# Kernel optimization log

Measured on AMD Instinct MI355X. Metric: run time of the kernel, lower is better.

Reference implementation:

```python
import jax, jax.numpy as jnp
import numpy as np

N = 100000   # nodes
E = 1600000  # edges (avg degree 16)
F_IN, F_HID, F_OUT = 64, 64, 16


def setup_inputs() -> dict:
    key = jax.random.key(0)
    ks = jax.random.split(key, 10)
    features = jax.random.normal(ks[0], (N, F_IN), dtype=jnp.float32)
    src = jax.random.randint(ks[1], (E,), 0, N, dtype=jnp.int32)
    dst = jax.random.randint(ks[2], (E,), 0, N, dtype=jnp.int32)
    # Xavier-uniform weights, zero bias (matches nn.init in the module)
    def xavier(k, fan_in, fan_out):
        lim = np.sqrt(6.0 / (fan_in + fan_out))
        return jax.random.uniform(k, (fan_in, fan_out), jnp.float32, -lim, lim)
    return {
        "features": features,
        "W1": xavier(ks[3], F_IN, F_HID), "b1": jnp.zeros((F_HID,), jnp.float32),
        "W2": xavier(ks[4], F_HID, F_HID), "b2": jnp.zeros((F_HID,), jnp.float32),
        "W3": xavier(ks[5], F_HID, F_OUT), "b3": jnp.zeros((F_OUT,), jnp.float32),
        "src": src, "dst": dst,
    }


def pairnorm_scs(x):
    # PairNorm 'PN-SCS', scale=1
    col_mean = x.mean(axis=0)                                    # [F]
    rownorm = jnp.sqrt(1e-6 + jnp.sum(x * x, axis=1, keepdims=True))  # [N,1]
    return x / rownorm - col_mean


def graph_conv(h, src, dst, W, b):
    # copy_u('h','m') + sum reduce over edges, plus self-loop
    agg = jax.ops.segment_sum(h[src], dst, num_segments=N) + h   # [N,F]
    return agg @ W + b


def reference(features, W1, b1, W2, b2, W3, b3, src, dst):
    h = features
    for W, b in ((W1, b1), (W2, b2)):
        h = pairnorm_scs(h)
        h = jax.nn.relu(graph_conv(h, src, dst, W, b))
        # dropout p=0.0 -> identity
    return graph_conv(h, src, dst, W3, b3)
```

## Files before the change

### kernel.cpp

```cpp
#include <hip/hip_runtime.h>
#include <hip/hip_fp8.h>


#define NHB 128

__device__ __forceinline__ unsigned short f2bf(float f) {
  unsigned u = __builtin_bit_cast(unsigned, f);
  u += 0x7FFFu + ((u >> 16) & 1u);
  return (unsigned short)(u >> 16);
}
__device__ __forceinline__ float bf2f(unsigned short h) {
  return __builtin_bit_cast(float, ((unsigned)h) << 16);
}
__device__ __forceinline__ float rlane(float v, int k) {
  return __builtin_bit_cast(
      float, __builtin_amdgcn_readlane(__builtin_bit_cast(int, v), k));
}
__device__ __forceinline__ unsigned char f2fp8(float f) {
  __hip_fp8_e4m3 t(f);
  return (unsigned char)t.__x;
}
__device__ __forceinline__ float fp8tof(unsigned v) {
#if __has_builtin(__builtin_amdgcn_cvt_f32_fp8)
  return __builtin_amdgcn_cvt_f32_fp8((int)v, 0);
#else
  const unsigned h = ((v << 8) & 0x8000u) | ((v << 7) & 0x3f80u);
  __half_raw hr; hr.x = (unsigned short)h;
  return (float)__half(hr) * 256.0f;
#endif
}

__global__ __launch_bounds__(256) void prelude_kernel(
    const int* __restrict__ dst, int* __restrict__ cntA, int E,
    const float* __restrict__ x, float* __restrict__ cs, int n4) {
  __shared__ int lc[NHB];
  __shared__ float lds[16][64];
  const int t = threadIdx.x;
  if (t < NHB) lc[t] = 0;
  __syncthreads();
  const int stride = gridDim.x * blockDim.x;
  for (int e = blockIdx.x * blockDim.x + t; e < E; e += stride)
    atomicAdd(&lc[__builtin_nontemporal_load(&dst[e]) >> 10], 1);

  float s0 = 0.f, s1 = 0.f, s2 = 0.f, s3 = 0.f;
  for (int i = blockIdx.x * blockDim.x + t; i < n4; i += stride) {
    float4 v = ((const float4*)x)[i];
    s0 += v.x; s1 += v.y; s2 += v.z; s3 += v.w;
  }
  const int r = t >> 4;
  const int cq = (t & 15) * 4;
  lds[r][cq + 0] = s0; lds[r][cq + 1] = s1; lds[r][cq + 2] = s2; lds[r][cq + 3] = s3;
  __syncthreads();
  if (t < NHB && lc[t]) atomicAdd(&cntA[t], lc[t]);
  if (t < 64) {
    float tot = 0.f;
    #pragma unroll
    for (int rr = 0; rr < 16; ++rr) tot += lds[rr][t];
    unsafeAtomicAdd(&cs[t], tot);
  }
}

__global__ __launch_bounds__(256) void matnorm_kernel(
    const float* x, const float* __restrict__ W,
    const float* __restrict__ cs, unsigned char* __restrict__ z,
    int N, float invN) {
  const int lane = threadIdx.x & 63;
  const int wid  = blockIdx.x * (blockDim.x >> 6) + (threadIdx.x >> 6);
  const int nw   = gridDim.x * (blockDim.x >> 6);

  float w[64];
  float cm0 = 0.f, cm1 = 0.f, cm2 = 0.f, cm3 = 0.f;
  #pragma unroll
  for (int k = 0; k < 64; k += 4) {
    w[k + 0] = W[(k + 0) * 64 + lane];
    w[k + 1] = W[(k + 1) * 64 + lane];
    w[k + 2] = W[(k + 2) * 64 + lane];
    w[k + 3] = W[(k + 3) * 64 + lane];
    cm0 = fmaf(cs[k + 0], w[k + 0], cm0);
    cm1 = fmaf(cs[k + 1], w[k + 1], cm1);
    cm2 = fmaf(cs[k + 2], w[k + 2], cm2);
    cm3 = fmaf(cs[k + 3], w[k + 3], cm3);
  }
  const float cm = ((cm0 + cm1) + (cm2 + cm3)) * invN;

  for (int row = wid; row < N; row += nw) {
    const float xv = x[(size_t)row * 64 + lane];
    float ss = xv * xv;
    #pragma unroll
    for (int m = 1; m < 64; m <<= 1) ss += __shfl_xor(ss, m, 64);
    const float rinv = 1.0f / sqrtf(1e-6f + ss);
    float a0 = 0.f, a1 = 0.f, a2 = 0.f, a3 = 0.f;
    #pragma unroll
    for (int k = 0; k < 64; k += 4) {
      a0 = fmaf(rlane(xv, k + 0), w[k + 0], a0);
      a1 = fmaf(rlane(xv, k + 1), w[k + 1], a1);
      a2 = fmaf(rlane(xv, k + 2), w[k + 2], a2);
      a3 = fmaf(rlane(xv, k + 3), w[k + 3], a3);
    }
    const float acc = (a0 + a1) + (a2 + a3);
    z[(size_t)row * 64 + lane] = f2fp8(acc * rinv - cm);
  }
}

__global__ __launch_bounds__(256) void matnorm2_kernel(
    const float* x, const float* __restrict__ W,
    float* __restrict__ cs, unsigned char* __restrict__ z, int N) {
  __shared__ float lred[4][64];
  const int lane = threadIdx.x & 63;
  const int wv   = threadIdx.x >> 6;
  const int wid  = blockIdx.x * (blockDim.x >> 6) + wv;
  const int nw   = gridDim.x * (blockDim.x >> 6);

  float w[64];
  #pragma unroll
  for (int k = 0; k < 64; k += 4) {
    w[k + 0] = W[(k + 0) * 64 + lane];
    w[k + 1] = W[(k + 1) * 64 + lane];
    w[k + 2] = W[(k + 2) * 64 + lane];
    w[k + 3] = W[(k + 3) * 64 + lane];
  }

  float csum = 0.f;
  for (int row = wid; row < N; row += nw) {
    const float xv = x[(size_t)row * 64 + lane];
    csum += xv;
    float ss = xv * xv;
    #pragma unroll
    for (int m = 1; m < 64; m <<= 1) ss += __shfl_xor(ss, m, 64);
    const float rinv = 1.0f / sqrtf(1e-6f + ss);
    float a0 = 0.f, a1 = 0.f, a2 = 0.f, a3 = 0.f;
    #pragma unroll
    for (int k = 0; k < 64; k += 4) {
      a0 = fmaf(rlane(xv, k + 0), w[k + 0], a0);
      a1 = fmaf(rlane(xv, k + 1), w[k + 1], a1);
      a2 = fmaf(rlane(xv, k + 2), w[k + 2], a2);
      a3 = fmaf(rlane(xv, k + 3), w[k + 3], a3);
    }
    const float acc = (a0 + a1) + (a2 + a3);
    z[(size_t)row * 64 + lane] = f2fp8(acc * rinv);
  }
  lred[wv][lane] = csum;
  __syncthreads();
  if (threadIdx.x < 64) {
    const float tot = lred[0][lane] + lred[1][lane] + lred[2][lane] + lred[3][lane];
    unsafeAtomicAdd(&cs[lane], tot);
  }
}

__global__ void cm2_kernel(const float* __restrict__ cs,
                           const float* __restrict__ W,
                           float* __restrict__ cm2, float invN) {
  const int m = threadIdx.x;
  float a0 = 0.f, a1 = 0.f, a2 = 0.f, a3 = 0.f;
  #pragma unroll
  for (int k = 0; k < 64; k += 4) {
    a0 = fmaf(cs[k + 0], W[(k + 0) * 64 + m], a0);
    a1 = fmaf(cs[k + 1], W[(k + 1) * 64 + m], a1);
    a2 = fmaf(cs[k + 2], W[(k + 2) * 64 + m], a2);
    a3 = fmaf(cs[k + 3], W[(k + 3) * 64 + m], a3);
  }
  cm2[m] = ((a0 + a1) + (a2 + a3)) * invN;
}


__global__ void scanA_kernel(const int* __restrict__ cntA,
                             int* __restrict__ baseA, int* __restrict__ curA,
                             int NHI) {
  __shared__ int s[NHB];
  const int t = threadIdx.x;
  const int v = (t < NHI) ? cntA[t] : 0;
  s[t] = v;
  __syncthreads();
  int acc = v;
  for (int off = 1; off < NHB; off <<= 1) {
    const int add = (t >= off) ? s[t - off] : 0;
    __syncthreads();
    acc += add;
    s[t] = acc;
    __syncthreads();
  }
  const int excl = acc - v;
  if (t < NHI) { baseA[t] = excl; curA[t] = excl; }
  if (t == NHI - 1) baseA[NHI] = acc;
}

#define TILE 2048
#define CAPA 48
__global__ __launch_bounds__(256) void scatterA_kernel(
    const int* __restrict__ src, const int* __restrict__ dst,
    int* __restrict__ curA, unsigned* __restrict__ ppack, int E) {
  __shared__ unsigned lpk[NHB][CAPA];
  __shared__ int lcnt[NHB], lbase[NHB];
  const int t = threadIdx.x;
  if (t < NHB) lcnt[t] = 0;
  __syncthreads();
  const int ntiles = (E + TILE - 1) / TILE;
  for (int tile = blockIdx.x; tile < ntiles; tile += gridDim.x) {
    const int base = tile * TILE;
    #pragma unroll
    for (int j = 0; j < TILE / 256; ++j) {
      const int e = base + j * 256 + t;
      if (e < E) {
        const int d = __builtin_nontemporal_load(&dst[e]);
        const int s = __builtin_nontemporal_load(&src[e]);
        const unsigned pw = ((unsigned)s << 10) | ((unsigned)d & 1023u);
        const int p = d >> 10;
        const int slot = atomicAdd(&lcnt[p], 1);
        if (slot < CAPA) lpk[p][slot] = pw;
        else ppack[atomicAdd(&curA[p], 1)] = pw;
      }
    }
    __syncthreads();
    if (t < NHB) {
      int c = lcnt[t]; if (c > CAPA) c = CAPA;
      lbase[t] = c ? atomicAdd(&curA[t], c) : 0;
      lcnt[t] = c;
    }
    __syncthreads();
    for (int p = 0; p < NHB; ++p) {
      const int c = lcnt[p];
      if (t < c) ppack[lbase[p] + t] = lpk[p][t];
    }
    __syncthreads();
    if (t < NHB) lcnt[t] = 0;
    __syncthreads();
  }
}

__global__ __launch_bounds__(1024) void fillsort_kernel(
    const unsigned* __restrict__ ppack, const int* __restrict__ baseA,
    int* __restrict__ rowstart, int* __restrict__ csr, int N, int E) {
  __shared__ int hist[1024];
  __shared__ int bs[1024];
  const int t = threadIdx.x;
  const int h = blockIdx.x;
  const int nlo = h << 10;
  const int elo = baseA[h], ehi = baseA[h + 1];

  hist[t] = 0;
  __syncthreads();

  int e = elo + t;
  for (; e + 3 * 1024 < ehi; e += 4 * 1024) {
    const unsigned p0 = ppack[e], p1 = ppack[e + 1024],
                   p2 = ppack[e + 2048], p3 = ppack[e + 3072];
    atomicAdd(&hist[p0 & 1023u], 1); atomicAdd(&hist[p1 & 1023u], 1);
    atomicAdd(&hist[p2 & 1023u], 1); atomicAdd(&hist[p3 & 1023u], 1);
  }
  for (; e < ehi; e += 1024) atomicAdd(&hist[ppack[e] & 1023u], 1);
  __syncthreads();

  const int c = hist[t];
  bs[t] = c;
  __syncthreads();
  for (int off = 1; off < 1024; off <<= 1) {
    const int v = (t >= off) ? bs[t - off] : 0;
    __syncthreads();
    bs[t] += v;
    __syncthreads();
  }
  const int excl = bs[t] - c;

  hist[t] = excl;
  const int n0 = nlo + t;
  if (n0 < N) rowstart[n0] = elo + excl;
  if (h == 0 && t == 0) rowstart[N] = E;
  __syncthreads();

  e = elo + t;
  for (; e + 3 * 1024 < ehi; e += 4 * 1024) {
    const unsigned p0 = ppack[e],        p1 = ppack[e + 1024];
    const unsigned p2 = ppack[e + 2048], p3 = ppack[e + 3072];
    csr[elo + atomicAdd(&hist[p0 & 1023u], 1)] = (int)(p0 >> 10);
    csr[elo + atomicAdd(&hist[p1 & 1023u], 1)] = (int)(p1 >> 10);
    csr[elo + atomicAdd(&hist[p2 & 1023u], 1)] = (int)(p2 >> 10);
    csr[elo + atomicAdd(&hist[p3 & 1023u], 1)] = (int)(p3 >> 10);
  }
  for (; e < ehi; e += 1024) {
    const unsigned p = ppack[e];
    csr[elo + atomicAdd(&hist[p & 1023u], 1)] = (int)(p >> 10);
  }
}

__global__ __launch_bounds__(256) void gather64_kernel(
    const unsigned char* __restrict__ z, const float* __restrict__ b,
    const int* __restrict__ rowstart, const int* __restrict__ csr,
    float* __restrict__ agg, int N) {
  const int lane = threadIdx.x & 63;
  int node = blockIdx.x * (blockDim.x >> 6) + (threadIdx.x >> 6);
  if (node >= N) return;
  node = __builtin_amdgcn_readfirstlane(node);
  const int start = rowstart[node];
  const int end   = rowstart[node + 1];
  const unsigned char hs = z[(size_t)node * 64 + lane];
  float a0 = 0.f, a1 = 0.f, a2 = 0.f, a3 = 0.f;
  int e = start;
  for (; e + 16 <= end; e += 16) {
    unsigned char h[16];
    #pragma unroll
    for (int j = 0; j < 16; ++j) h[j] = z[(size_t)csr[e + j] * 64 + lane];
    #pragma unroll
    for (int j = 0; j < 16; j += 4) {
      a0 += fp8tof(h[j + 0]); a1 += fp8tof(h[j + 1]);
      a2 += fp8tof(h[j + 2]); a3 += fp8tof(h[j + 3]);
    }
  }
  for (; e + 4 <= end; e += 4) {
    unsigned char h[4];
    #pragma unroll
    for (int j = 0; j < 4; ++j) h[j] = z[(size_t)csr[e + j] * 64 + lane];
    a0 += fp8tof(h[0]); a1 += fp8tof(h[1]); a2 += fp8tof(h[2]); a3 += fp8tof(h[3]);
  }
  for (; e < end; ++e) a0 += fp8tof(z[(size_t)csr[e] * 64 + lane]);
  const float sum = (a0 + a1) + (a2 + a3);
  agg[(size_t)node * 64 + lane] = fmaxf(fp8tof(hs) + b[lane] + sum, 0.f);
}

__global__ __launch_bounds__(256) void gather_l2_kernel(
    const unsigned char* __restrict__ z2, const float* __restrict__ b2,
    const float* __restrict__ W3, const float* __restrict__ cm2,
    const int* __restrict__ rowstart, const int* __restrict__ csr,
    unsigned char* __restrict__ z3, int N) {
  const int lane = threadIdx.x & 63;
  int node = blockIdx.x * (blockDim.x >> 6) + (threadIdx.x >> 6);
  if (node >= N) return;
  node = __builtin_amdgcn_readfirstlane(node);
  float4 w4[4];
  #pragma unroll
  for (int q = 0; q < 4; ++q)
    w4[q] = ((const float4*)(W3 + lane * 16))[q];
  const float cml = cm2[lane];

  const int start = rowstart[node];
  const int end   = rowstart[node + 1];
  const unsigned char hs = z2[(size_t)node * 64 + lane];
  float a0 = 0.f, a1 = 0.f, a2 = 0.f, a3 = 0.f;
  int e = start;
  for (; e + 16 <= end; e += 16) {
    unsigned char h[16];
    #pragma unroll
    for (int j = 0; j < 16; ++j) h[j] = z2[(size_t)csr[e + j] * 64 + lane];
    #pragma unroll
    for (int j = 0; j < 16; j += 4) {
      a0 += fp8tof(h[j + 0]); a1 += fp8tof(h[j + 1]);
      a2 += fp8tof(h[j + 2]); a3 += fp8tof(h[j + 3]);
    }
  }
  for (; e + 4 <= end; e += 4) {
    unsigned char h[4];
    #pragma unroll
    for (int j = 0; j < 4; ++j) h[j] = z2[(size_t)csr[e + j] * 64 + lane];
    a0 += fp8tof(h[0]); a1 += fp8tof(h[1]); a2 += fp8tof(h[2]); a3 += fp8tof(h[3]);
  }
  for (; e < end; ++e) a0 += fp8tof(z2[(size_t)csr[e] * 64 + lane]);
  const float sum = (a0 + a1) + (a2 + a3);
  const float corr = (float)(end - start + 1) * cml;
  const float o = fmaxf(fp8tof(hs) + b2[lane] + sum - corr, 0.f);

  float p[16];
  #pragma unroll
  for (int q = 0; q < 4; ++q) {
    p[4 * q + 0] = o * w4[q].x;
    p[4 * q + 1] = o * w4[q].y;
    p[4 * q + 2] = o * w4[q].z;
    p[4 * q + 3] = o * w4[q].w;
  }
  {
    const bool up = (lane & 1);
    #pragma unroll
    for (int m = 0; m < 8; ++m) {
      const float mine = up ? p[m + 8] : p[m];
      const float give = up ? p[m] : p[m + 8];
      p[m] = mine + __shfl_xor(give, 1, 64);
    }
  }
  {
    const bool up = (lane & 2);
    #pragma unroll
    for (int m = 0; m < 4; ++m) {
      const float mine = up ? p[m + 4] : p[m];
      const float give = up ? p[m] : p[m + 4];
      p[m] = mine + __shfl_xor(give, 2, 64);
    }
  }
  {
    const bool up = (lane & 4);
    #pragma unroll
    for (int m = 0; m < 2; ++m) {
      const float mine = up ? p[m + 2] : p[m];
      const float give = up ? p[m] : p[m + 2];
      p[m] = mine + __shfl_xor(give, 4, 64);
    }
  }
  {
    const bool up = (lane & 8);
    const float mine = up ? p[1] : p[0];
    const float give = up ? p[0] : p[1];
    p[0] = mine + __shfl_xor(give, 8, 64);
  }
  p[0] += __shfl_xor(p[0], 16, 64);
  p[0] += __shfl_xor(p[0], 32, 64);

  if (lane < 16) {
    const int j = ((lane & 1) << 3) | ((lane & 2) << 1) |
                  ((lane & 4) >> 1) | ((lane & 8) >> 3);
    z3[(size_t)node * 16 + j] = f2fp8(p[0]);
  }
}

__global__ __launch_bounds__(256) void gather16_kernel(
    const unsigned char* __restrict__ z3, const float* __restrict__ b3,
    const int* __restrict__ rowstart, const int* __restrict__ csr,
    float* __restrict__ out, int N) {
  const int lane = threadIdx.x & 63;
  const int f = lane & 15;
  const int g = lane >> 4;
  int node = blockIdx.x * (blockDim.x >> 6) + (threadIdx.x >> 6);
  if (node >= N) return;
  node = __builtin_amdgcn_readfirstlane(node);
  const int start = rowstart[node];
  const int end   = rowstart[node + 1];
  float acc0 = 0.f, acc1 = 0.f;
  int e = start + g;
  for (; e + 4 < end; e += 8) {
    acc0 += fp8tof(z3[(size_t)csr[e] * 16 + f]);
    acc1 += fp8tof(z3[(size_t)csr[e + 4] * 16 + f]);
  }
  if (e < end) acc0 += fp8tof(z3[(size_t)csr[e] * 16 + f]);
  float acc = acc0 + acc1;
  acc += __shfl_xor(acc, 16, 64);
  acc += __shfl_xor(acc, 32, 64);
  if (lane < 16)
    out[(size_t)node * 16 + f] = fp8tof(z3[(size_t)node * 16 + f]) + b3[f] + acc;
}

extern "C" void kernel_launch(void* const* d_in, const int* in_sizes, int n_in,
                              void* d_out, int out_size, void* d_ws, size_t ws_size,
                              hipStream_t stream) {
  const float* feat = (const float*)d_in[0];
  const float* W1 = (const float*)d_in[1];
  const float* b1 = (const float*)d_in[2];
  const float* W2 = (const float*)d_in[3];
  const float* b2 = (const float*)d_in[4];
  const float* W3 = (const float*)d_in[5];
  const float* b3 = (const float*)d_in[6];
  const int* src = (const int*)d_in[7];
  const int* dst = (const int*)d_in[8];
  const int N = in_sizes[0] / 64;
  const int E = in_sizes[7];
  float* out = (float*)d_out;

  float* B            = (float*)d_ws;
  unsigned char* zb   = (unsigned char*)(B + (size_t)N * 64);
  unsigned char* z3b  = zb + (size_t)N * 64;
  int* cntA  = (int*)(z3b + (size_t)N * 16);
  float* cs1 = (float*)(cntA + NHB);
  float* cs2 = cs1 + 64;
  float* cm2w = cs2 + 64;
  int* baseA    = (int*)(cm2w + 64);
  int* curA     = baseA + NHB + 1;
  int* rowstart = curA + NHB;
  int* csr      = rowstart + N + 1;
  unsigned* ppack = (unsigned*)zb;

  const int NHI = (N + 1023) >> 10;
  const int node_blocks = (N + 3) / 4;
  const float invN = 1.0f / (float)N;

  hipMemsetAsync(cntA, 0, (NHB + 128) * sizeof(int), stream);
  prelude_kernel<<<512, 256, 0, stream>>>(dst, cntA, E, feat, cs1, N * 16);
  scanA_kernel<<<1, NHB, 0, stream>>>(cntA, baseA, curA, NHI);
  scatterA_kernel<<<512, 256, 0, stream>>>(src, dst, curA, ppack, E);
  fillsort_kernel<<<NHI, 1024, 0, stream>>>(ppack, baseA, rowstart, csr, N, E);

  matnorm_kernel<<<1024, 256, 0, stream>>>(feat, W1, cs1, zb, N, invN);
  gather64_kernel<<<node_blocks, 256, 0, stream>>>(zb, b1, rowstart, csr, B, N);

  matnorm2_kernel<<<1024, 256, 0, stream>>>(B, W2, cs2, zb, N);
  cm2_kernel<<<1, 64, 0, stream>>>(cs2, W2, cm2w, invN);
  gather_l2_kernel<<<node_blocks, 256, 0, stream>>>(zb, b2, W3, cm2w, rowstart,
                                                    csr, z3b, N);

  gather16_kernel<<<node_blocks, 256, 0, stream>>>(z3b, b3, rowstart, csr, out, N);
}
```

Before: 386.9 us.

## Process two nodes per wavefront with 2-byte fp8 gathers and shuffled CSR indices

The 64-wide gather kernels for layers 1 and 2 now split each wavefront into two halves that each handle one node. Each lane loads two fp8 features at once and converts them with the packed fp8-to-float conversion. Neighbor indices are loaded cooperatively once per 32 edges and broadcast with shuffles, replacing a per-lane scalar CSR read per edge. This halves the wave count and cuts scalar index traffic. In exchange, the two nodes share a loop bounded by the larger degree, so the smaller-degree half does masked extra iterations. The layer-3 projection reduction is adjusted for two features per lane.

```diff
diff --git a/kernel.cpp b/kernel.cpp
--- a/kernel.cpp
+++ b/kernel.cpp
@@ -3,6 +3,8 @@
 
 
 #define NHB 128
+
+typedef float floatx2 __attribute__((ext_vector_type(2)));
 
 __device__ __forceinline__ unsigned short f2bf(float f) {
   unsigned u = __builtin_bit_cast(unsigned, f);
@@ -27,6 +29,13 @@
   const unsigned h = ((v << 8) & 0x8000u) | ((v << 7) & 0x3f80u);
   __half_raw hr; hr.x = (unsigned short)h;
   return (float)__half(hr) * 256.0f;
+#endif
+}
+__device__ __forceinline__ floatx2 fp8x2tof(unsigned short p) {
+#if __has_builtin(__builtin_amdgcn_cvt_pk_f32_fp8)
+  return __builtin_amdgcn_cvt_pk_f32_fp8((int)(unsigned)p, false);
+#else
+  floatx2 r; r.x = fp8tof(p & 0xffu); r.y = fp8tof(p >> 8); return r;
 #endif
 }
 
@@ -287,33 +296,84 @@
     const int* __restrict__ rowstart, const int* __restrict__ csr,
     float* __restrict__ agg, int N) {
   const int lane = threadIdx.x & 63;
-  int node = blockIdx.x * (blockDim.x >> 6) + (threadIdx.x >> 6);
-  if (node >= N) return;
-  node = __builtin_amdgcn_readfirstlane(node);
-  const int start = rowstart[node];
-  const int end   = rowstart[node + 1];
-  const unsigned char hs = z[(size_t)node * 64 + lane];
-  float a0 = 0.f, a1 = 0.f, a2 = 0.f, a3 = 0.f;
-  int e = start;
-  for (; e + 16 <= end; e += 16) {
-    unsigned char h[16];
-    #pragma unroll
-    for (int j = 0; j < 16; ++j) h[j] = z[(size_t)csr[e + j] * 64 + lane];
-    #pragma unroll
-    for (int j = 0; j < 16; j += 4) {
-      a0 += fp8tof(h[j + 0]); a1 += fp8tof(h[j + 1]);
-      a2 += fp8tof(h[j + 2]); a3 += fp8tof(h[j + 3]);
-    }
-  }
-  for (; e + 4 <= end; e += 4) {
-    unsigned char h[4];
-    #pragma unroll
-    for (int j = 0; j < 4; ++j) h[j] = z[(size_t)csr[e + j] * 64 + lane];
-    a0 += fp8tof(h[0]); a1 += fp8tof(h[1]); a2 += fp8tof(h[2]); a3 += fp8tof(h[3]);
-  }
-  for (; e < end; ++e) a0 += fp8tof(z[(size_t)csr[e] * 64 + lane]);
-  const float sum = (a0 + a1) + (a2 + a3);
-  agg[(size_t)node * 64 + lane] = fmaxf(fp8tof(hs) + b[lane] + sum, 0.f);
+  const int h    = lane >> 5;
+  const int il   = lane & 31;
+  const int f0   = il << 1;
+  const int pair = blockIdx.x * (blockDim.x >> 6) + (threadIdx.x >> 6);
+  const int n0 = pair << 1;
+  if (n0 >= N) return;
+  const int node = n0 + h;
+  const bool hv = (node < N);
+  const int start = hv ? rowstart[node] : 0;
+  const int end   = hv ? rowstart[node + 1] : 0;
+  const int deg   = end - start;
+  const int degA = __builtin_amdgcn_readfirstlane(deg);
+  const int degB = __builtin_amdgcn_readlane(deg, 32);
+  const int maxdeg = degA > degB ? degA : degB;
+
+  const unsigned char* zp = z + f0;
+  const unsigned short sv =
+      hv ? *(const unsigned short*)(zp + (size_t)node * 64) : (unsigned short)0;
+
+  float a00 = 0.f, a01 = 0.f, a10 = 0.f, a11 = 0.f;
+  for (int w0 = 0; w0 < maxdeg; w0 += 32) {
+    const int ei = start + w0 + il;
+    const int safe = (ei < end) ? ei : (end > start ? end - 1 : 0);
+    const int cidx = csr[safe];
+    const int rem = maxdeg - w0;
+    const int nloc = rem < 32 ? rem : 32;
+    int j0 = 0;
+    for (; j0 + 16 <= nloc; j0 += 16) {
+      int idx[16];
+      #pragma unroll
+      for (int j = 0; j < 16; ++j)
+        idx[j] = __shfl(cidx, (h << 5) + j0 + j, 64);
+      unsigned short hh[16];
+      #pragma unroll
+      for (int j = 0; j < 16; ++j)
+        hh[j] = *(const unsigned short*)(zp + (size_t)(unsigned)idx[j] * 64u);
+      #pragma unroll
+      for (int j = 0; j < 16; ++j) {
+        const unsigned short m = (w0 + j0 + j < deg) ? hh[j] : (unsigned short)0;
+        const floatx2 v = fp8x2tof(m);
+        if (j & 1) { a10 += v.x; a11 += v.y; }
+        else       { a00 += v.x; a01 += v.y; }
+      }
+    }
+    for (; j0 + 4 <= nloc; j0 += 4) {
+      int idx[4];
+      #pragma unroll
+      for (int j = 0; j < 4; ++j)
+        idx[j] = __shfl(cidx, (h << 5) + j0 + j, 64);
+      unsigned short hh[4];
+      #pragma unroll
+      for (int j = 0; j < 4; ++j)
+        hh[j] = *(const unsigned short*)(zp + (size_t)(unsigned)idx[j] * 64u);
+      #pragma unroll
+      for (int j = 0; j < 4; ++j) {
+        const unsigned short m = (w0 + j0 + j < deg) ? hh[j] : (unsigned short)0;
+        const floatx2 v = fp8x2tof(m);
+        if (j & 1) { a10 += v.x; a11 += v.y; }
+        else       { a00 += v.x; a01 += v.y; }
+      }
+    }
+    for (; j0 < nloc; ++j0) {
+      const int idx = __shfl(cidx, (h << 5) + j0, 64);
+      const unsigned short hh =
+          *(const unsigned short*)(zp + (size_t)(unsigned)idx * 64u);
+      const unsigned short m = (w0 + j0 < deg) ? hh : (unsigned short)0;
+      const floatx2 v = fp8x2tof(m);
+      a00 += v.x; a01 += v.y;
+    }
+  }
+  if (hv) {
+    const floatx2 sf = fp8x2tof(sv);
+    const float2 bb = *(const float2*)(b + f0);
+    float2 st;
+    st.x = fmaxf(sf.x + bb.x + a00 + a10, 0.f);
+    st.y = fmaxf(sf.y + bb.y + a01 + a11, 0.f);
+    *(float2*)(agg + (size_t)node * 64 + f0) = st;
+  }
 }
 
 __global__ __launch_bounds__(256) void gather_l2_kernel(
@@ -322,48 +382,100 @@
     const int* __restrict__ rowstart, const int* __restrict__ csr,
     unsigned char* __restrict__ z3, int N) {
   const int lane = threadIdx.x & 63;
-  int node = blockIdx.x * (blockDim.x >> 6) + (threadIdx.x >> 6);
-  if (node >= N) return;
-  node = __builtin_amdgcn_readfirstlane(node);
-  float4 w4[4];
+  const int h    = lane >> 5;
+  const int il   = lane & 31;
+  const int f0   = il << 1;
+  const int pair = blockIdx.x * (blockDim.x >> 6) + (threadIdx.x >> 6);
+  const int n0 = pair << 1;
+  if (n0 >= N) return;
+  float4 wA[4], wB[4];
   #pragma unroll
-  for (int q = 0; q < 4; ++q)
-    w4[q] = ((const float4*)(W3 + lane * 16))[q];
-  const float cml = cm2[lane];
-
-  const int start = rowstart[node];
-  const int end   = rowstart[node + 1];
-  const unsigned char hs = z2[(size_t)node * 64 + lane];
-  float a0 = 0.f, a1 = 0.f, a2 = 0.f, a3 = 0.f;
-  int e = start;
-  for (; e + 16 <= end; e += 16) {
-    unsigned char h[16];
-    #pragma unroll
-    for (int j = 0; j < 16; ++j) h[j] = z2[(size_t)csr[e + j] * 64 + lane];
-    #pragma unroll
-    for (int j = 0; j < 16; j += 4) {
-      a0 += fp8tof(h[j + 0]); a1 += fp8tof(h[j + 1]);
-      a2 += fp8tof(h[j + 2]); a3 += fp8tof(h[j + 3]);
-    }
-  }
-  for (; e + 4 <= end; e += 4) {
-    unsigned char h[4];
-    #pragma unroll
-    for (int j = 0; j < 4; ++j) h[j] = z2[(size_t)csr[e + j] * 64 + lane];
-    a0 += fp8tof(h[0]); a1 += fp8tof(h[1]); a2 += fp8tof(h[2]); a3 += fp8tof(h[3]);
-  }
-  for (; e < end; ++e) a0 += fp8tof(z2[(size_t)csr[e] * 64 + lane]);
-  const float sum = (a0 + a1) + (a2 + a3);
-  const float corr = (float)(end - start + 1) * cml;
-  const float o = fmaxf(fp8tof(hs) + b2[lane] + sum - corr, 0.f);
+  for (int q = 0; q < 4; ++q) {
+    wA[q] = ((const float4*)(W3 + f0 * 16))[q];
+    wB[q] = ((const float4*)(W3 + (f0 + 1) * 16))[q];
+  }
+  const int node = n0 + h;
+  const bool hvd = (node < N);
+  const int start = hvd ? rowstart[node] : 0;
+  const int end   = hvd ? rowstart[node + 1] : 0;
+  const int deg   = end - start;
+  const int degA = __builtin_amdgcn_readfirstlane(deg);
+  const int degB = __builtin_amdgcn_readlane(deg, 32);
+  const int maxdeg = degA > degB ? degA : degB;
+
+  const unsigned char* zp = z2 + f0;
+  const unsigned short sv =
+      hvd ? *(const unsigned short*)(zp + (size_t)node * 64) : (unsigned short)0;
+
+  float a00 = 0.f, a01 = 0.f, a10 = 0.f, a11 = 0.f;
+  for (int w0 = 0; w0 < maxdeg; w0 += 32) {
+    const int ei = start + w0 + il;
+    const int safe = (ei < end) ? ei : (end > start ? end - 1 : 0);
+    const int cidx = csr[safe];
+    const int rem = maxdeg - w0;
+    const int nloc = rem < 32 ? rem : 32;
+    int j0 = 0;
+    for (; j0 + 16 <= nloc; j0 += 16) {
+      int idx[16];
+      #pragma unroll
+      for (int j = 0; j < 16; ++j)
+        idx[j] = __shfl(cidx, (h << 5) + j0 + j, 64);
+      unsigned short hh[16];
+      #pragma unroll
+      for (int j = 0; j < 16; ++j)
+        hh[j] = *(const unsigned short*)(zp + (size_t)(unsigned)idx[j] * 64u);
+      #pragma unroll
+      for (int j = 0; j < 16; ++j) {
+        const unsigned short m = (w0 + j0 + j < deg) ? hh[j] : (unsigned short)0;
+        const floatx2 v = fp8x2tof(m);
+        if (j & 1) { a10 += v.x; a11 += v.y; }
+        else       { a00 += v.x; a01 += v.y; }
+      }
+    }
+    for (; j0 + 4 <= nloc; j0 += 4) {
+      int idx[4];
+      #pragma unroll
+      for (int j = 0; j < 4; ++j)
+        idx[j] = __shfl(cidx, (h << 5) + j0 + j, 64);
+      unsigned short hh[4];
+      #pragma unroll
+      for (int j = 0; j < 4; ++j)
+        hh[j] = *(const unsigned short*)(zp + (size_t)(unsigned)idx[j] * 64u);
+      #pragma unroll
+      for (int j = 0; j < 4; ++j) {
+        const unsigned short m = (w0 + j0 + j < deg) ? hh[j] : (unsigned short)0;
+        const floatx2 v = fp8x2tof(m);
+        if (j & 1) { a10 += v.x; a11 += v.y; }
+        else       { a00 += v.x; a01 += v.y; }
+      }
+    }
+    for (; j0 < nloc; ++j0) {
+      const int idx = __shfl(cidx, (h << 5) + j0, 64);
+      const unsigned short hh =
+          *(const unsigned short*)(zp + (size_t)(unsigned)idx * 64u);
+      const unsigned short m = (w0 + j0 < deg) ? hh : (unsigned short)0;
+      const floatx2 v = fp8x2tof(m);
+      a00 += v.x; a01 += v.y;
+    }
+  }
+
+  float o0 = 0.f, o1 = 0.f;
+  if (hvd) {
+    const floatx2 sf = fp8x2tof(sv);
+    const float2 bb = *(const float2*)(b2 + f0);
+    const float2 cc = *(const float2*)(cm2 + f0);
+    const float dp1 = (float)(deg + 1);
+    o0 = fmaxf(sf.x + bb.x + (a00 + a10) - dp1 * cc.x, 0.f);
+    o1 = fmaxf(sf.y + bb.y + (a01 + a11) - dp1 * cc.y, 0.f);
+  }
 
   float p[16];
   #pragma unroll
   for (int q = 0; q < 4; ++q) {
-    p[4 * q + 0] = o * w4[q].x;
-    p[4 * q + 1] = o * w4[q].y;
-    p[4 * q + 2] = o * w4[q].z;
-    p[4 * q + 3] = o * w4[q].w;
+    p[4 * q + 0] = fmaf(o0, wA[q].x, o1 * wB[q].x);
+    p[4 * q + 1] = fmaf(o0, wA[q].y, o1 * wB[q].y);
+    p[4 * q + 2] = fmaf(o0, wA[q].z, o1 * wB[q].z);
+    p[4 * q + 3] = fmaf(o0, wA[q].w, o1 * wB[q].w);
   }
   {
     const bool up = (lane & 1);
@@ -399,11 +511,10 @@
     p[0] = mine + __shfl_xor(give, 8, 64);
   }
   p[0] += __shfl_xor(p[0], 16, 64);
-  p[0] += __shfl_xor(p[0], 32, 64);
-
-  if (lane < 16) {
-    const int j = ((lane & 1) << 3) | ((lane & 2) << 1) |
-                  ((lane & 4) >> 1) | ((lane & 8) >> 3);
+
+  if (hvd && il < 16) {
+    const int j = ((il & 1) << 3) | ((il & 2) << 1) |
+                  ((il & 4) >> 1) | ((il & 8) >> 3);
     z3[(size_t)node * 16 + j] = f2fp8(p[0]);
   }
 }
@@ -465,6 +576,8 @@
 
   const int NHI = (N + 1023) >> 10;
   const int node_blocks = (N + 3) / 4;
+  const int npairs = (N + 1) / 2;
+  const int pair_blocks = (npairs + 3) / 4;
   const float invN = 1.0f / (float)N;
 
   hipMemsetAsync(cntA, 0, (NHB + 128) * sizeof(int), stream);
@@ -474,11 +587,11 @@
   fillsort_kernel<<<NHI, 1024, 0, stream>>>(ppack, baseA, rowstart, csr, N, E);
 
   matnorm_kernel<<<1024, 256, 0, stream>>>(feat, W1, cs1, zb, N, invN);
-  gather64_kernel<<<node_blocks, 256, 0, stream>>>(zb, b1, rowstart, csr, B, N);
+  gather64_kernel<<<pair_blocks, 256, 0, stream>>>(zb, b1, rowstart, csr, B, N);
 
   matnorm2_kernel<<<1024, 256, 0, stream>>>(B, W2, cs2, zb, N);
   cm2_kernel<<<1, 64, 0, stream>>>(cs2, W2, cm2w, invN);
-  gather_l2_kernel<<<node_blocks, 256, 0, stream>>>(zb, b2, W3, cm2w, rowstart,
+  gather_l2_kernel<<<pair_blocks, 256, 0, stream>>>(zb, b2, W3, cm2w, rowstart,
                                                     csr, z3b, N);
 
   gather16_kernel<<<node_blocks, 256, 0, stream>>>(z3b, b3, rowstart, csr, out, N);
```

Measured after the change: 387.0 us. About the same (+0.0%).

## Process two nodes per wavefront in layer-1 gather with packed fp8 loads

Applied to the files above, without the earlier changes.

The layer-1 gather kernel now assigns two destination nodes to each 64-lane wavefront, with each half-wave handling one node and each lane loading two fp8 features as a 16-bit word. Neighbor indices are loaded cooperatively, one per lane, and broadcast with shuffles instead of every lane reading the same CSR entry, and a packed fp8-to-f32 conversion is used. This halves the wavefront count and the per-edge scalar index loads. The cost is that both halves loop to the larger of the two degrees with masked loads, which wastes work when the degrees differ.

```diff
diff --git a/kernel.cpp b/kernel.cpp
--- a/kernel.cpp
+++ b/kernel.cpp
@@ -3,6 +3,8 @@
 
 
 #define NHB 128
+
+typedef float floatx2 __attribute__((ext_vector_type(2)));
 
 __device__ __forceinline__ unsigned short f2bf(float f) {
   unsigned u = __builtin_bit_cast(unsigned, f);
@@ -27,6 +29,13 @@
   const unsigned h = ((v << 8) & 0x8000u) | ((v << 7) & 0x3f80u);
   __half_raw hr; hr.x = (unsigned short)h;
   return (float)__half(hr) * 256.0f;
+#endif
+}
+__device__ __forceinline__ floatx2 fp8x2tof(unsigned short p) {
+#if __has_builtin(__builtin_amdgcn_cvt_pk_f32_fp8)
+  return __builtin_amdgcn_cvt_pk_f32_fp8((int)(unsigned)p, false);
+#else
+  floatx2 r; r.x = fp8tof(p & 0xffu); r.y = fp8tof(p >> 8); return r;
 #endif
 }
 
@@ -287,33 +296,84 @@
     const int* __restrict__ rowstart, const int* __restrict__ csr,
     float* __restrict__ agg, int N) {
   const int lane = threadIdx.x & 63;
-  int node = blockIdx.x * (blockDim.x >> 6) + (threadIdx.x >> 6);
-  if (node >= N) return;
-  node = __builtin_amdgcn_readfirstlane(node);
-  const int start = rowstart[node];
-  const int end   = rowstart[node + 1];
-  const unsigned char hs = z[(size_t)node * 64 + lane];
-  float a0 = 0.f, a1 = 0.f, a2 = 0.f, a3 = 0.f;
-  int e = start;
-  for (; e + 16 <= end; e += 16) {
-    unsigned char h[16];
-    #pragma unroll
-    for (int j = 0; j < 16; ++j) h[j] = z[(size_t)csr[e + j] * 64 + lane];
-    #pragma unroll
-    for (int j = 0; j < 16; j += 4) {
-      a0 += fp8tof(h[j + 0]); a1 += fp8tof(h[j + 1]);
-      a2 += fp8tof(h[j + 2]); a3 += fp8tof(h[j + 3]);
-    }
-  }
-  for (; e + 4 <= end; e += 4) {
-    unsigned char h[4];
-    #pragma unroll
-    for (int j = 0; j < 4; ++j) h[j] = z[(size_t)csr[e + j] * 64 + lane];
-    a0 += fp8tof(h[0]); a1 += fp8tof(h[1]); a2 += fp8tof(h[2]); a3 += fp8tof(h[3]);
-  }
-  for (; e < end; ++e) a0 += fp8tof(z[(size_t)csr[e] * 64 + lane]);
-  const float sum = (a0 + a1) + (a2 + a3);
-  agg[(size_t)node * 64 + lane] = fmaxf(fp8tof(hs) + b[lane] + sum, 0.f);
+  const int h    = lane >> 5;
+  const int il   = lane & 31;
+  const int f0   = il << 1;
+  const int pair = blockIdx.x * (blockDim.x >> 6) + (threadIdx.x >> 6);
+  const int n0 = pair << 1;
+  if (n0 >= N) return;
+  const int node = n0 + h;
+  const bool hv = (node < N);
+  const int start = hv ? rowstart[node] : 0;
+  const int end   = hv ? rowstart[node + 1] : 0;
+  const int deg   = end - start;
+  const int degA = __builtin_amdgcn_readfirstlane(deg);
+  const int degB = __builtin_amdgcn_readlane(deg, 32);
+  const int maxdeg = degA > degB ? degA : degB;
+
+  const unsigned char* zp = z + f0;
+  const unsigned short sv =
+      hv ? *(const unsigned short*)(zp + (size_t)node * 64) : (unsigned short)0;
+
+  float a00 = 0.f, a01 = 0.f, a10 = 0.f, a11 = 0.f;
+  for (int w0 = 0; w0 < maxdeg; w0 += 32) {
+    const int ei = start + w0 + il;
+    const int safe = (ei < end) ? ei : (end > start ? end - 1 : 0);
+    const int cidx = csr[safe];
+    const int rem = maxdeg - w0;
+    const int nloc = rem < 32 ? rem : 32;
+    int j0 = 0;
+    for (; j0 + 16 <= nloc; j0 += 16) {
+      int idx[16];
+      #pragma unroll
+      for (int j = 0; j < 16; ++j)
+        idx[j] = __shfl(cidx, (h << 5) + j0 + j, 64);
+      unsigned short hh[16];
+      #pragma unroll
+      for (int j = 0; j < 16; ++j)
+        hh[j] = *(const unsigned short*)(zp + (size_t)(unsigned)idx[j] * 64u);
+      #pragma unroll
+      for (int j = 0; j < 16; ++j) {
+        const unsigned short m = (w0 + j0 + j < deg) ? hh[j] : (unsigned short)0;
+        const floatx2 v = fp8x2tof(m);
+        if (j & 1) { a10 += v.x; a11 += v.y; }
+        else       { a00 += v.x; a01 += v.y; }
+      }
+    }
+    for (; j0 + 4 <= nloc; j0 += 4) {
+      int idx[4];
+      #pragma unroll
+      for (int j = 0; j < 4; ++j)
+        idx[j] = __shfl(cidx, (h << 5) + j0 + j, 64);
+      unsigned short hh[4];
+      #pragma unroll
+      for (int j = 0; j < 4; ++j)
+        hh[j] = *(const unsigned short*)(zp + (size_t)(unsigned)idx[j] * 64u);
+      #pragma unroll
+      for (int j = 0; j < 4; ++j) {
+        const unsigned short m = (w0 + j0 + j < deg) ? hh[j] : (unsigned short)0;
+        const floatx2 v = fp8x2tof(m);
+        if (j & 1) { a10 += v.x; a11 += v.y; }
+        else       { a00 += v.x; a01 += v.y; }
+      }
+    }
+    for (; j0 < nloc; ++j0) {
+      const int idx = __shfl(cidx, (h << 5) + j0, 64);
+      const unsigned short hh =
+          *(const unsigned short*)(zp + (size_t)(unsigned)idx * 64u);
+      const unsigned short m = (w0 + j0 < deg) ? hh : (unsigned short)0;
+      const floatx2 v = fp8x2tof(m);
+      a00 += v.x; a01 += v.y;
+    }
+  }
+  if (hv) {
+    const floatx2 sf = fp8x2tof(sv);
+    const float2 bb = *(const float2*)(b + f0);
+    float2 st;
+    st.x = fmaxf(sf.x + bb.x + a00 + a10, 0.f);
+    st.y = fmaxf(sf.y + bb.y + a01 + a11, 0.f);
+    *(float2*)(agg + (size_t)node * 64 + f0) = st;
+  }
 }
 
 __global__ __launch_bounds__(256) void gather_l2_kernel(
@@ -465,6 +525,8 @@
 
   const int NHI = (N + 1023) >> 10;
   const int node_blocks = (N + 3) / 4;
+  const int npairs = (N + 1) / 2;
+  const int pair_blocks = (npairs + 3) / 4;
   const float invN = 1.0f / (float)N;
 
   hipMemsetAsync(cntA, 0, (NHB + 128) * sizeof(int), stream);
@@ -474,7 +536,7 @@
   fillsort_kernel<<<NHI, 1024, 0, stream>>>(ppack, baseA, rowstart, csr, N, E);
 
   matnorm_kernel<<<1024, 256, 0, stream>>>(feat, W1, cs1, zb, N, invN);
-  gather64_kernel<<<node_blocks, 256, 0, stream>>>(zb, b1, rowstart, csr, B, N);
+  gather64_kernel<<<pair_blocks, 256, 0, stream>>>(zb, b1, rowstart, csr, B, N);
 
   matnorm2_kernel<<<1024, 256, 0, stream>>>(B, W2, cs2, zb, N);
   cm2_kernel<<<1, 64, 0, stream>>>(cs2, W2, cm2w, invN);
```

Result: faster. 371.6 us (-4.0%).
